# Performance work log

Measured on AMD Instinct MI355X. Metric: run time of the kernel, lower is better.

Reference implementation:

```python
import jax, jax.numpy as jnp
import numpy as np

N = 50000   # nodes
E = 400000  # edges
D = 256     # embedding_dimension
R = 2       # num_relations
NE = 2      # num experts
OUT = 256   # output_size
NEG_SLOPE = 0.01  # nn.LeakyReLU default


def setup_inputs() -> dict:
    key = jax.random.key(0)
    ks = jax.random.split(key, 18)
    s = 0.05
    inp = {
        "des": jax.random.normal(ks[0], (N, 128), jnp.float32),
        "tweet": jax.random.normal(ks[1], (N, 64), jnp.float32),
        "num_prop": jax.random.normal(ks[2], (N, 32), jnp.float32),
        "cat_prop": jax.random.normal(ks[3], (N, 32), jnp.float32),
        "edge_index": jax.random.randint(ks[4], (2, E), 0, N, jnp.int64),
        "edge_type": jax.random.randint(ks[5], (E,), 0, R, jnp.int64),
        # linear_relu_input
        "W_in": jax.random.normal(ks[6], (D, D), jnp.float32) * s,
        "b_in": jnp.zeros((D,), jnp.float32),
        # RGCNConv (shared across the two calls)
        "W_rel": jax.random.normal(ks[7], (R, D, D), jnp.float32) * s,
        "W_root": jax.random.normal(ks[8], (D, D), jnp.float32) * s,
        "b_rgcn": jnp.zeros((D,), jnp.float32),
        # MoE gate + experts (MLP: D -> D -> OUT)
        "w_gate": jax.random.normal(ks[9], (D, NE), jnp.float32) * s,
        "We1": jax.random.normal(ks[10], (NE, D, D), jnp.float32) * s,
        "be1": jnp.zeros((NE, D), jnp.float32),
        "We2": jax.random.normal(ks[11], (NE, D, OUT), jnp.float32) * s,
        "be2": jnp.zeros((NE, OUT), jnp.float32),
    }
    return inp


def _rgcn(x, W_rel, W_root, b, src, dst, edge_type):
    # per-relation node transform, then gather per edge; mean-aggregate per (node, relation)
    h = jnp.einsum('nd,rdh->rnh', x, W_rel)          # (R, N, D)
    msg = h[edge_type, src]                           # (E, D)
    seg = dst * R + edge_type                         # combined (node, relation) segment id
    sums = jax.ops.segment_sum(msg, seg, num_segments=N * R)
    cnt = jax.ops.segment_sum(jnp.ones((E,), msg.dtype), seg, num_segments=N * R)
    agg = sums / jnp.maximum(cnt, 1.0)[:, None]       # per-relation mean (0 if no edges)
    agg = agg.reshape(N, R, -1).sum(axis=1)           # sum over relations
    return x @ W_root + b + agg


def _moe(x, w_gate, We1, be1, We2, be2, k=1):
    # clean (eval) top-k gating: softmax over the top-k logits, scattered into zeros
    logits = x @ w_gate                               # (N, NE)
    top_vals, top_idx = jax.lax.top_k(logits, k)
    gate_vals = jax.nn.softmax(top_vals, axis=-1)     # k=1 -> weight 1.0
    gates = jnp.zeros_like(logits).at[jnp.arange(x.shape[0])[:, None], top_idx].set(gate_vals)
    # compute all experts densely (zero gates annihilate unselected experts)
    h1 = jnp.einsum('nd,edh->enh', x, We1) + be1[:, None, :]
    h1 = jnp.where(h1 >= 0, h1, NEG_SLOPE * h1)       # LeakyReLU
    ye = jnp.einsum('enh,eho->eno', h1, We2) + be2[:, None, :]
    return jnp.einsum('ne,eno->no', gates, ye)


def reference(des, tweet, num_prop, cat_prop, edge_index, edge_type,
              W_in, b_in, W_rel, W_root, b_rgcn, w_gate, We1, be1, We2, be2):
    src, dst = edge_index[0], edge_index[1]
    x = jnp.concatenate((des, tweet, num_prop, cat_prop), axis=1)  # (N, D)
    x = jax.nn.selu(x @ W_in + b_in)
    x = _rgcn(x, W_rel, W_root, b_rgcn, src, dst, edge_type)
    # dropout is identity in eval mode
    x = _rgcn(x, W_rel, W_root, b_rgcn, src, dst, edge_type)
    y = _moe(x, w_gate, We1, be1, We2, be2, k=1)
    return y
```

## Files before the change

kernel.cpp:

```cpp
#include <hip/hip_runtime.h>
#include <cstddef>

static constexpr int N_NODES = 50000;
static constexpr int N_EDGES = 400000;
static constexpr int D = 256;
static constexpr int R = 2;
static constexpr int M_PAD = 50048;
static constexpr int CAP = 32;
static constexpr int NSEG = N_NODES * R;

typedef _Float16 f16x8 __attribute__((ext_vector_type(8)));
typedef float f32x4 __attribute__((ext_vector_type(4)));

__device__ __forceinline__ unsigned short f2h(float f) {
    _Float16 h = (_Float16)f;
    return *(unsigned short*)&h;
}
__device__ __forceinline__ float h2f(unsigned short u) {
    _Float16 h = *(_Float16*)&u;
    return (float)h;
}

#define GLOAD16(g, l)                                                          \
    __builtin_amdgcn_global_load_lds(                                          \
        (const __attribute__((address_space(1))) void*)(g),                    \
        (__attribute__((address_space(3))) void*)(l), 16, 0, 0)

struct SSlab { const float* x; int xstr; int kstart; int mload; };
struct SArgs {
    SSlab sl[4];
    int nslab;
    const unsigned short* wt;
    int Ktot;
    int M;
    const float* bias;
    void* out;
};

template<int ACT>
__global__ __launch_bounds__(256, 2)
void sgemm(SArgs a) {
    __shared__ unsigned short As[2][128 * 32];
    __shared__ unsigned short Bs[2][128 * 32];
    const int tid  = threadIdx.x;
    const int wave = tid >> 6, lane = tid & 63;
    const int wm = wave >> 1, wn = wave & 1;
    const int row0 = blockIdx.x * 128;
    const int n0   = blockIdx.y * 128;

    const int arow  = tid >> 1;
    const int ahalf = tid & 1;
    const int br_   = tid >> 2;
    const int bg_   = tid & 3;

    const int gk   = lane >> 4;
    const int frow = lane & 15;
    const int fslot = (gk ^ ((frow >> 1) & 3)) << 3;

    f32x4 acc0[4][4] = {};
    f32x4 accC[4][4] = {};

    for (int ks = 0; ks < a.Ktot; ks += 32) {
        int s = a.nslab - 1;
        while (s > 0 && ks < a.sl[s].kstart) --s;
        const float* xb = a.sl[s].x;
        const int xstr  = a.sl[s].xstr;
        const int kloc  = ks - a.sl[s].kstart;
        const int mload = a.sl[s].mload;

        float ev[16];
        {
            const int gr = row0 + arow;
            if (gr < mload) {
                const float* ap = xb + (size_t)gr * xstr + kloc + ahalf * 16;
                *(float4*)&ev[0]  = ((const float4*)ap)[0];
                *(float4*)&ev[4]  = ((const float4*)ap)[1];
                *(float4*)&ev[8]  = ((const float4*)ap)[2];
                *(float4*)&ev[12] = ((const float4*)ap)[3];
            } else {
                #pragma unroll
                for (int j = 0; j < 16; ++j) ev[j] = 0.f;
            }
        }

        __syncthreads();

        #pragma unroll
        for (int p = 0; p < 2; ++p) {
            #pragma unroll
            for (int q = 0; q < 2; ++q) {
                const int r = q * 64 + br_;
                const int gsrc = (bg_ ^ ((r >> 1) & 3)) << 3;
                GLOAD16(a.wt + (size_t)p * 256 * a.Ktot + (size_t)(n0 + r) * a.Ktot + ks + gsrc,
                        &Bs[p][(q * 64 + wave * 16) * 32]);
            }
        }

        {
            const int sswz = (arow >> 1) & 3;
            #pragma unroll
            for (int g = 0; g < 2; ++g) {
                union { f16x8 v; _Float16 h[8]; } p1, p2;
                #pragma unroll
                for (int j = 0; j < 8; ++j) {
                    const float v = ev[g * 8 + j];
                    const _Float16 h1 = (_Float16)v;
                    const float r1 = (v - (float)h1) * 2048.0f;
                    p1.h[j] = h1; p2.h[j] = (_Float16)r1;
                }
                const int slot = ((ahalf * 2 + g) ^ sswz) << 3;
                *(f16x8*)&As[0][arow * 32 + slot] = p1.v;
                *(f16x8*)&As[1][arow * 32 + slot] = p2.v;
            }
        }

        __syncthreads();

        f16x8 bq[4][2];
        #pragma unroll
        for (int n = 0; n < 4; ++n) {
            const int rr = wn * 64 + n * 16 + frow;
            #pragma unroll
            for (int p = 0; p < 2; ++p)
                bq[n][p] = *(const f16x8*)&Bs[p][rr * 32 + fslot];
        }
        #pragma unroll
        for (int m = 0; m < 4; ++m) {
            const int rr = wm * 64 + m * 16 + frow;
            const f16x8 a1 = *(const f16x8*)&As[0][rr * 32 + fslot];
            const f16x8 a2 = *(const f16x8*)&As[1][rr * 32 + fslot];
            #pragma unroll
            for (int n = 0; n < 4; ++n) {
                acc0[m][n] = __builtin_amdgcn_mfma_f32_16x16x32_f16(a1, bq[n][0], acc0[m][n], 0, 0, 0);
                accC[m][n] = __builtin_amdgcn_mfma_f32_16x16x32_f16(a1, bq[n][1], accC[m][n], 0, 0, 0);
                accC[m][n] = __builtin_amdgcn_mfma_f32_16x16x32_f16(a2, bq[n][0], accC[m][n], 0, 0, 0);
            }
        }
    }

    const int erow = (lane >> 4) * 4;
    const int ecol = lane & 15;
    #pragma unroll
    for (int m = 0; m < 4; ++m) {
        #pragma unroll
        for (int r = 0; r < 4; ++r) {
            const int grow = row0 + wm * 64 + m * 16 + erow + r;
            if (grow >= a.M) continue;
            #pragma unroll
            for (int n = 0; n < 4; ++n) {
                const int gcol = n0 + wn * 64 + n * 16 + ecol;
                float v = acc0[m][n][r] + accC[m][n][r] * (1.0f / 2048.0f) + a.bias[gcol];
                if (ACT == 1) {
                    const float scale = 1.0507009873554804934f;
                    const float alpha = 1.6732632423543772848f;
                    v = (v > 0.f) ? scale * v : scale * alpha * (expf(v) - 1.f);
                }
                ((float*)a.out)[(size_t)grow * 256 + gcol] = v;
            }
        }
    }
}

struct HSlab { const void* x; int xstr; int kstart; };
struct HArgs {
    HSlab sl[3];
    int nslab;
    const unsigned short* wt;
    int Ktot, M;
    const float* bias;
    const int* sel;
    const int* perm;
    const int* c01;
    void* out;
    int ldc;
};

template<int ACT, bool MASK, bool SELB, bool OUTF16, bool A32, bool EZ, bool PERM>
__global__ __launch_bounds__(256, 2)
void hgemm(HArgs a) {
    __shared__ unsigned short As[128 * 64];
    __shared__ unsigned short Bs[128 * 64];
    const int tid  = threadIdx.x;
    const int wave = tid >> 6, lane = tid & 63;
    const int wm = wave >> 1, wn = wave & 1;
    const int row0 = blockIdx.x * 128;
    const int n0   = blockIdx.y * 128;
    const int ex   = EZ ? (int)blockIdx.z : 0;
    const unsigned short* wt = a.wt + (size_t)ex * 65536;
    const float* bias = a.bias + ex * 256;

    int cntE = 0, base = 0;
    if (PERM) {
        const int c0 = a.c01[0];
        cntE = (ex == 0) ? c0 : a.M - c0;
        base = (ex == 0) ? 0 : c0;
        if (row0 >= cntE) return;
    }

    const int srow = lane >> 3;
    const int scol = ((lane & 7) ^ (lane >> 3)) << 3;
    const int arow  = tid >> 1;
    const int ahalf = tid & 1;

    f32x4 acc[4][4] = {};

    for (int k0 = 0; k0 < a.Ktot; k0 += 64) {
        int s = a.nslab - 1;
        while (s > 0 && k0 < a.sl[s].kstart) --s;
        const int kloc = k0 - a.sl[s].kstart;
        const int xstr = a.sl[s].xstr;

        float ev[32];
        if (A32) {
            const float* xp = (const float*)a.sl[s].x;
            const float* ap = xp + (size_t)(row0 + arow) * xstr + kloc + ahalf * 32;
            #pragma unroll
            for (int q = 0; q < 8; ++q)
                *(float4*)&ev[q * 4] = ((const float4*)ap)[q];
        }

        __syncthreads();

        if (!A32) {
            const unsigned short* xp = (const unsigned short*)a.sl[s].x;
            #pragma unroll
            for (int i = 0; i < 4; ++i) {
                const int r = wave * 32 + i * 8;
                int lr = row0 + r + srow;
                if (PERM) lr = a.perm[base + (lr < cntE ? lr : cntE - 1)];
                GLOAD16(xp + (size_t)lr * xstr + kloc + scol, &As[r * 64]);
            }
        }
        #pragma unroll
        for (int i = 0; i < 4; ++i) {
            const int r = wave * 32 + i * 8;
            GLOAD16(wt + (size_t)(n0 + r + srow) * a.Ktot + k0 + scol, &Bs[r * 64]);
        }
        if (A32) {
            #pragma unroll
            for (int gi = 0; gi < 4; ++gi) {
                const int sgr = ahalf * 4 + gi;
                union { f16x8 v; _Float16 h[8]; } pk;
                #pragma unroll
                for (int j = 0; j < 8; ++j) pk.h[j] = (_Float16)ev[gi * 8 + j];
                *(f16x8*)&As[arow * 64 + ((sgr ^ (arow & 7)) << 3)] = pk.v;
            }
        }

        __syncthreads();

        #pragma unroll
        for (int kk = 0; kk < 2; ++kk) {
            const int gkk = kk * 4 + (lane >> 4);
            f16x8 af[4], bfr[4];
            #pragma unroll
            for (int m = 0; m < 4; ++m) {
                const int rr = wm * 64 + m * 16 + (lane & 15);
                af[m] = *(const f16x8*)&As[rr * 64 + ((gkk ^ (rr & 7)) << 3)];
            }
            #pragma unroll
            for (int n = 0; n < 4; ++n) {
                const int rr = wn * 64 + n * 16 + (lane & 15);
                bfr[n] = *(const f16x8*)&Bs[rr * 64 + ((gkk ^ (rr & 7)) << 3)];
            }
            #pragma unroll
            for (int m = 0; m < 4; ++m)
                #pragma unroll
                for (int n = 0; n < 4; ++n)
                    acc[m][n] = __builtin_amdgcn_mfma_f32_16x16x32_f16(
                        af[m], bfr[n], acc[m][n], 0, 0, 0);
        }
    }

    const int erow = (lane >> 4) * 4;
    const int ecol = lane & 15;
    #pragma unroll
    for (int m = 0; m < 4; ++m) {
        #pragma unroll
        for (int r = 0; r < 4; ++r) {
            const int grow = row0 + wm * 64 + m * 16 + erow + r;
            if (PERM) { if (grow >= cntE) continue; }
            else      { if (grow >= a.M) continue; }
            const int orow = PERM ? a.perm[base + grow] : grow;
            int sv = 0;
            if (MASK || SELB) sv = a.sel[orow];
            #pragma unroll
            for (int n = 0; n < 4; ++n) {
                const int gcol = n0 + wn * 64 + n * 16 + ecol;
                const float b = SELB ? a.bias[sv * 256 + gcol] : bias[gcol];
                float v = acc[m][n][r] + b;
                if (ACT == 2) v = (v >= 0.f) ? v : 0.01f * v;
                if (MASK && sv != ex) v = 0.f;
                const size_t oidx = (size_t)orow * a.ldc + ((EZ && !PERM) ? ex * 256 : 0) + gcol;
                if (OUTF16) ((unsigned short*)a.out)[oidx] = f2h(v);
                else        ((float*)a.out)[oidx] = v;
            }
        }
    }
}

__global__ __launch_bounds__(256)
void csr_build(const int* __restrict__ ei, const int* __restrict__ et,
               int* cnt, int* slots) {
    const int e = blockIdx.x * 256 + threadIdx.x;
    if (e >= N_EDGES) return;
    const int src = ei[e];
    const int dst = ei[N_EDGES + e];
    const int seg = dst * R + et[e];
    const int slot = atomicAdd(&cnt[seg], 1);
    if (slot < CAP) slots[(size_t)seg * CAP + slot] = src;
}

__global__ __launch_bounds__(256)
void aggregate(const float* __restrict__ X, const int* __restrict__ cnt,
               const int* __restrict__ slots, float* __restrict__ Ab,
               int seg0, int nseg) {
    const int w = blockIdx.x * 4 + (threadIdx.x >> 6);
    if (w >= nseg) return;
    const int lane = threadIdx.x & 63;
    const int s = seg0 + w;
    const int m = min(cnt[s], CAP);
    const int* sl = slots + (size_t)s * CAP;
    float4 acc = make_float4(0.f, 0.f, 0.f, 0.f);
    for (int i = 0; i < m; ++i) {
        const float4 v = *(const float4*)(X + (size_t)sl[i] * 256 + lane * 4);
        acc.x += v.x; acc.y += v.y; acc.z += v.z; acc.w += v.w;
    }
    const float inv = (m > 0) ? 1.0f / (float)m : 0.0f;
    acc.x *= inv; acc.y *= inv; acc.z *= inv; acc.w *= inv;
    *(float4*)(Ab + (size_t)(w >> 1) * 512 + (w & 1) * 256 + lane * 4) = acc;
}

__global__ __launch_bounds__(256)
void agg_h(const unsigned short* __restrict__ Xh, const int* __restrict__ cnt,
           const int* __restrict__ slots, unsigned short* __restrict__ Abh) {
    const int w = blockIdx.x * 4 + (threadIdx.x >> 6);
    if (w >= NSEG) return;
    const int lane = threadIdx.x & 63;
    const int m = min(cnt[w], CAP);
    const int* sl = slots + (size_t)w * CAP;
    float ac[4] = {};
    for (int i = 0; i < m; ++i) {
        const ushort4 v = *(const ushort4*)(Xh + (size_t)sl[i] * 256 + lane * 4);
        ac[0] += h2f(v.x); ac[1] += h2f(v.y); ac[2] += h2f(v.z); ac[3] += h2f(v.w);
    }
    const float inv = (m > 0) ? 1.0f / (float)m : 0.0f;
    ushort4 o = make_ushort4(f2h(ac[0] * inv), f2h(ac[1] * inv),
                             f2h(ac[2] * inv), f2h(ac[3] * inv));
    *(ushort4*)(Abh + (size_t)(w >> 1) * 512 + (w & 1) * 256 + lane * 4) = o;
}

__global__ __launch_bounds__(256)
void fold1(const float* __restrict__ W_root, const float* __restrict__ W_rel,
           const float* __restrict__ b_rg, const float* __restrict__ wg,
           float* __restrict__ wfold, float* __restrict__ c3) {
    const int idx = blockIdx.x * 256 + threadIdx.x;
    if (idx < 1536) {
        const int d = idx / 6, jj = idx % 6, c = jj >> 1, j = jj & 1;
        const float* row = (c == 0) ? W_root + (size_t)d * 256
                                    : W_rel + (size_t)(c - 1) * 65536 + (size_t)d * 256;
        float s = 0.f;
        for (int e = 0; e < 256; ++e) s += row[e] * wg[e * 2 + j];
        wfold[idx] = s;
    } else if (idx < 1538) {
        const int j = idx - 1536;
        float s = 0.f;
        for (int e = 0; e < 256; ++e) s += b_rg[e] * wg[e * 2 + j];
        c3[j] = s;
    }
}

__global__ __launch_bounds__(256)
void fold2(const float* __restrict__ W_root, const float* __restrict__ W_rel,
           const float* __restrict__ b_rg, const float* __restrict__ wfold,
           float* __restrict__ W6, float* __restrict__ cb) {
    const int idx = blockIdx.x * 256 + threadIdx.x;
    if (idx < 4608) {
        const int k = idx / 6, j = idx % 6;
        const float* row = (k < 256) ? W_root + (size_t)k * 256
                                     : W_rel + (size_t)(k - 256) * 256;
        float s = 0.f;
        for (int d = 0; d < 256; ++d) s += row[d] * wfold[d * 6 + j];
        W6[idx] = s;
    } else if (idx < 4614) {
        const int j = idx - 4608;
        float s = 0.f;
        for (int d = 0; d < 256; ++d) s += b_rg[d] * wfold[d * 6 + j];
        cb[j] = s;
    }
}

__global__ __launch_bounds__(256)
void vu_kernel(const float* __restrict__ X1, const float* __restrict__ Ab,
               const float* __restrict__ W6, float* __restrict__ VU, int M) {
    __shared__ float wl[768 * 6];
    for (int i = threadIdx.x; i < 768 * 6; i += 256) wl[i] = W6[i];
    __syncthreads();
    const int wave = threadIdx.x >> 6, lane = threadIdx.x & 63;
    const int n = blockIdx.x * 4 + wave;
    if (n >= M) return;
    const float4 xv = ((const float4*)(X1 + (size_t)n * 256))[lane];
    const float4 a0 = ((const float4*)(Ab + (size_t)n * 512))[lane];
    const float4 a1 = ((const float4*)(Ab + (size_t)n * 512))[lane + 64];
    const float xa[12] = {xv.x, xv.y, xv.z, xv.w, a0.x, a0.y, a0.z, a0.w,
                          a1.x, a1.y, a1.z, a1.w};
    float z[6] = {};
    #pragma unroll
    for (int t = 0; t < 3; ++t)
        #pragma unroll
        for (int i = 0; i < 4; ++i) {
            const int k = t * 256 + lane * 4 + i;
            #pragma unroll
            for (int j = 0; j < 6; ++j) z[j] = fmaf(xa[t * 4 + i], wl[k * 6 + j], z[j]);
        }
    #pragma unroll
    for (int off = 32; off; off >>= 1)
        #pragma unroll
        for (int j = 0; j < 6; ++j) z[j] += __shfl_down(z[j], off, 64);
    if (lane == 0) {
        #pragma unroll
        for (int j = 0; j < 6; ++j) VU[(size_t)n * 6 + j] = z[j];
    }
}

__global__ __launch_bounds__(256)
void u_gate(const float* __restrict__ VU, const int* __restrict__ cnt,
            const int* __restrict__ slots, const float* __restrict__ cb,
            const float* __restrict__ c3, int* __restrict__ sel, int M) {
    const int n = blockIdx.x * 256 + threadIdx.x;
    if (n >= M) return;
    float z0 = VU[(size_t)n * 6 + 0] + cb[0] + c3[0];
    float z1 = VU[(size_t)n * 6 + 1] + cb[1] + c3[1];
    #pragma unroll
    for (int r = 0; r < 2; ++r) {
        const int seg = n * 2 + r;
        const int m = min(cnt[seg], CAP);
        if (m > 0) {
            const int* sl = slots + (size_t)seg * CAP;
            float s0 = 0.f, s1 = 0.f;
            for (int i = 0; i < m; ++i) {
                const int src = sl[i];
                s0 += VU[(size_t)src * 6 + 2 + 2 * r];
                s1 += VU[(size_t)src * 6 + 3 + 2 * r];
            }
            const float inv = 1.0f / (float)m;
            z0 += s0 * inv + cb[2 + 2 * r];
            z1 += s1 * inv + cb[3 + 2 * r];
        }
    }
    sel[n] = (z1 > z0) ? 1 : 0;
}

__global__ __launch_bounds__(256)
void build_perm(const int* __restrict__ sel, int* __restrict__ perm, int* c01) {
    const int n = blockIdx.x * 256 + threadIdx.x;
    if (n >= N_NODES) return;
    if (sel[n] == 0) perm[atomicAdd(&c01[0], 1)] = n;
    else             perm[N_NODES - 1 - atomicAdd(&c01[1], 1)] = n;
}

__global__ __launch_bounds__(256)
void wconv2(const float* __restrict__ src, unsigned short* __restrict__ dst) {
    const int i = blockIdx.x * 256 + threadIdx.x;
    const int k = i >> 8, n = i & 255;
    const float v = src[i];
    const _Float16 h1 = (_Float16)v;
    const float r1 = (v - (float)h1) * 2048.0f;
    dst[(size_t)n * 256 + k] = f2h(v);
    dst[65536 + (size_t)n * 256 + k] = *(unsigned short*)&h1 == 0 ? f2h(r1) : f2h(r1);
}

struct WJH { const float* src[8]; unsigned short* dst[8]; int stride[8]; int koff[8]; };
__global__ __launch_bounds__(256)
void wconv_h(WJH j) {
    const int job = blockIdx.y;
    const int i = blockIdx.x * 256 + threadIdx.x;
    const int k = i >> 8, n = i & 255;
    j.dst[job][(size_t)n * j.stride[job] + j.koff[job] + k] = f2h(j.src[job][i]);
}

extern "C" void kernel_launch(void* const* d_in, const int* in_sizes, int n_in,
                              void* d_out, int out_size, void* d_ws, size_t ws_size,
                              hipStream_t stream) {
    const float* des    = (const float*)d_in[0];
    const float* twt    = (const float*)d_in[1];
    const float* nump   = (const float*)d_in[2];
    const float* catp   = (const float*)d_in[3];
    const int*   ei     = (const int*)d_in[4];
    const int*   et     = (const int*)d_in[5];
    const float* W_in   = (const float*)d_in[6];
    const float* b_in   = (const float*)d_in[7];
    const float* W_rel  = (const float*)d_in[8];
    const float* W_root = (const float*)d_in[9];
    const float* b_rg   = (const float*)d_in[10];
    const float* w_gate = (const float*)d_in[11];
    const float* We1    = (const float*)d_in[12];
    const float* be1    = (const float*)d_in[13];
    const float* We2    = (const float*)d_in[14];
    const float* be2    = (const float*)d_in[15];

    char* ws = (char*)d_ws;
    size_t off = 0;
    auto alloc = [&](size_t bytes) { char* p = ws + off; off += (bytes + 255) & ~(size_t)255; return p; };
    float* X1f  = (float*)alloc((size_t)M_PAD * 256 * 4);
    char*  regA = alloc((size_t)M_PAD * 512 * 4);
    unsigned short* X2h = (unsigned short*)alloc((size_t)M_PAD * 256 * 2);
    float* VU   = (float*)alloc((size_t)N_NODES * 6 * 4);
    int*   cnt  = (int*)alloc((size_t)NSEG * 4);
    int*   sel  = (int*)alloc((size_t)N_NODES * 4);
    int*   perm = (int*)alloc((size_t)N_NODES * 4);
    int*   c01  = (int*)alloc(256);
    int*   slots= (int*)alloc((size_t)NSEG * CAP * 4);
    unsigned short* wt_in2 = (unsigned short*)alloc((size_t)2 * 65536 * 2);
    unsigned short* wt_rg  = (unsigned short*)alloc((size_t)256 * 768 * 2);
    unsigned short* wt_e1  = (unsigned short*)alloc((size_t)2 * 65536 * 2);
    unsigned short* wt_e2  = (unsigned short*)alloc((size_t)2 * 65536 * 2);
    float* wfold = (float*)alloc(256 * 6 * 4);
    float* c3    = (float*)alloc(8);
    float* W6    = (float*)alloc(768 * 6 * 4);
    float* cb    = (float*)alloc(24);

    float* Ab1f = (float*)regA;
    unsigned short* Ab2h = (unsigned short*)regA;
    unsigned short* H    = (unsigned short*)(regA + (size_t)M_PAD * 512 * 2);
    unsigned short* X3h  = (unsigned short*)X1f;

    const dim3 blk(256);

    hipMemsetAsync(cnt, 0, (size_t)NSEG * 4, stream);
    hipMemsetAsync(c01, 0, 8, stream);
    csr_build<<<(N_EDGES + 255) / 256, blk, 0, stream>>>(ei, et, cnt, slots);
    wconv2<<<256, blk, 0, stream>>>(W_in, wt_in2);
    {
        WJH j{};
        j.src[0] = W_root;         j.dst[0] = wt_rg;         j.stride[0] = 768; j.koff[0] = 0;
        j.src[1] = W_rel;          j.dst[1] = wt_rg;         j.stride[1] = 768; j.koff[1] = 256;
        j.src[2] = W_rel + 65536;  j.dst[2] = wt_rg;         j.stride[2] = 768; j.koff[2] = 512;
        j.src[3] = We1;            j.dst[3] = wt_e1;         j.stride[3] = 256; j.koff[3] = 0;
        j.src[4] = We1 + 65536;    j.dst[4] = wt_e1 + 65536; j.stride[4] = 256; j.koff[4] = 0;
        j.src[5] = We2;            j.dst[5] = wt_e2;         j.stride[5] = 256; j.koff[5] = 0;
        j.src[6] = We2 + 65536;    j.dst[6] = wt_e2 + 65536; j.stride[6] = 256; j.koff[6] = 0;
        wconv_h<<<dim3(256, 7), blk, 0, stream>>>(j);
    }
    fold1<<<7, blk, 0, stream>>>(W_root, W_rel, b_rg, w_gate, wfold, c3);
    fold2<<<19, blk, 0, stream>>>(W_root, W_rel, b_rg, wfold, W6, cb);

    {
        SArgs g{};
        g.sl[0] = {des,  128, 0,   N_NODES};
        g.sl[1] = {twt,  64,  128, N_NODES};
        g.sl[2] = {nump, 32,  192, N_NODES};
        g.sl[3] = {catp, 32,  224, N_NODES};
        g.nslab = 4; g.wt = wt_in2; g.Ktot = 256; g.M = N_NODES;
        g.bias = b_in; g.out = X1f;
        hipLaunchKernelGGL((sgemm<1>), dim3(391, 2), blk, 0, stream, g);
    }

    aggregate<<<(NSEG + 3) / 4, blk, 0, stream>>>(X1f, cnt, slots, Ab1f, 0, NSEG);

    vu_kernel<<<(N_NODES + 3) / 4, blk, 0, stream>>>(X1f, Ab1f, W6, VU, N_NODES);
    u_gate<<<(N_NODES + 255) / 256, blk, 0, stream>>>(VU, cnt, slots, cb, c3, sel, N_NODES);
    build_perm<<<(N_NODES + 255) / 256, blk, 0, stream>>>(sel, perm, c01);

    {
        HArgs g{};
        g.sl[0] = {X1f,        256, 0};
        g.sl[1] = {Ab1f,       512, 256};
        g.sl[2] = {Ab1f + 256, 512, 512};
        g.nslab = 3; g.wt = wt_rg; g.Ktot = 768; g.M = N_NODES;
        g.bias = b_rg; g.out = X2h; g.ldc = 256;
        hipLaunchKernelGGL((hgemm<0, false, false, true, true, false, false>),
                           dim3(391, 2), blk, 0, stream, g);
    }

    agg_h<<<(NSEG + 3) / 4, blk, 0, stream>>>(X2h, cnt, slots, Ab2h);

    {
        HArgs g{};
        g.sl[0] = {X2h,        256, 0};
        g.sl[1] = {Ab2h,       512, 256};
        g.sl[2] = {Ab2h + 256, 512, 512};
        g.nslab = 3; g.wt = wt_rg; g.Ktot = 768; g.M = N_NODES;
        g.bias = b_rg; g.out = X3h; g.ldc = 256;
        hipLaunchKernelGGL((hgemm<0, false, false, true, false, false, false>),
                           dim3(391, 2), blk, 0, stream, g);
    }

    {
        HArgs g{};
        g.sl[0] = {X3h, 256, 0};
        g.nslab = 1; g.wt = wt_e1; g.Ktot = 256; g.M = N_NODES;
        g.bias = be1; g.perm = perm; g.c01 = c01; g.out = H; g.ldc = 256;
        hipLaunchKernelGGL((hgemm<2, false, false, true, false, true, true>),
                           dim3(391, 2, 2), blk, 0, stream, g);
    }

    {
        HArgs g{};
        g.sl[0] = {H, 256, 0};
        g.nslab = 1; g.wt = wt_e2; g.Ktot = 256; g.M = N_NODES;
        g.bias = be2; g.perm = perm; g.c01 = c01; g.out = d_out; g.ldc = 256;
        hipLaunchKernelGGL((hgemm<0, false, false, false, false, true, true>),
                           dim3(391, 2, 2), blk, 0, stream, g);
    }
}
```

Before: 476.6 us.

## Double-buffer LDS tiles in sgemm/hgemm and unroll gather aggregation by two

```diff
diff --git a/kernel.cpp b/kernel.cpp
--- a/kernel.cpp
+++ b/kernel.cpp
@@ -40,8 +40,8 @@
 template<int ACT>
 __global__ __launch_bounds__(256, 2)
 void sgemm(SArgs a) {
-    __shared__ unsigned short As[2][128 * 32];
-    __shared__ unsigned short Bs[2][128 * 32];
+    __shared__ unsigned short As[2][2][128 * 32];
+    __shared__ unsigned short Bs[2][2][128 * 32];
     const int tid  = threadIdx.x;
     const int wave = tid >> 6, lane = tid & 63;
     const int wm = wave >> 1, wn = wave & 1;
@@ -57,34 +57,28 @@
     const int frow = lane & 15;
     const int fslot = (gk ^ ((frow >> 1) & 3)) << 3;
 
-    f32x4 acc0[4][4] = {};
-    f32x4 accC[4][4] = {};
-
-    for (int ks = 0; ks < a.Ktot; ks += 32) {
+    const int NT = a.Ktot / 32;
+    float ev[16];
+
+    auto loadA = [&](int t) {
+        const int ks = t * 32;
         int s = a.nslab - 1;
         while (s > 0 && ks < a.sl[s].kstart) --s;
-        const float* xb = a.sl[s].x;
-        const int xstr  = a.sl[s].xstr;
-        const int kloc  = ks - a.sl[s].kstart;
-        const int mload = a.sl[s].mload;
-
-        float ev[16];
-        {
-            const int gr = row0 + arow;
-            if (gr < mload) {
-                const float* ap = xb + (size_t)gr * xstr + kloc + ahalf * 16;
-                *(float4*)&ev[0]  = ((const float4*)ap)[0];
-                *(float4*)&ev[4]  = ((const float4*)ap)[1];
-                *(float4*)&ev[8]  = ((const float4*)ap)[2];
-                *(float4*)&ev[12] = ((const float4*)ap)[3];
-            } else {
-                #pragma unroll
-                for (int j = 0; j < 16; ++j) ev[j] = 0.f;
-            }
-        }
-
-        __syncthreads();
-
+        const int gr = row0 + arow;
+        if (gr < a.sl[s].mload) {
+            const float* ap = a.sl[s].x + (size_t)gr * a.sl[s].xstr
+                              + (ks - a.sl[s].kstart) + ahalf * 16;
+            *(float4*)&ev[0]  = ((const float4*)ap)[0];
+            *(float4*)&ev[4]  = ((const float4*)ap)[1];
+            *(float4*)&ev[8]  = ((const float4*)ap)[2];
+            *(float4*)&ev[12] = ((const float4*)ap)[3];
+        } else {
+            #pragma unroll
+            for (int j = 0; j < 16; ++j) ev[j] = 0.f;
+        }
+    };
+    auto stageB = [&](int buf, int t) {
+        const int ks = t * 32;
         #pragma unroll
         for (int p = 0; p < 2; ++p) {
             #pragma unroll
@@ -92,29 +86,39 @@
                 const int r = q * 64 + br_;
                 const int gsrc = (bg_ ^ ((r >> 1) & 3)) << 3;
                 GLOAD16(a.wt + (size_t)p * 256 * a.Ktot + (size_t)(n0 + r) * a.Ktot + ks + gsrc,
-                        &Bs[p][(q * 64 + wave * 16) * 32]);
-            }
-        }
-
-        {
-            const int sswz = (arow >> 1) & 3;
-            #pragma unroll
-            for (int g = 0; g < 2; ++g) {
-                union { f16x8 v; _Float16 h[8]; } p1, p2;
-                #pragma unroll
-                for (int j = 0; j < 8; ++j) {
-                    const float v = ev[g * 8 + j];
-                    const _Float16 h1 = (_Float16)v;
-                    const float r1 = (v - (float)h1) * 2048.0f;
-                    p1.h[j] = h1; p2.h[j] = (_Float16)r1;
-                }
-                const int slot = ((ahalf * 2 + g) ^ sswz) << 3;
-                *(f16x8*)&As[0][arow * 32 + slot] = p1.v;
-                *(f16x8*)&As[1][arow * 32 + slot] = p2.v;
-            }
-        }
-
-        __syncthreads();
+                        &Bs[buf][p][(q * 64 + wave * 16) * 32]);
+            }
+        }
+    };
+    auto writeA = [&](int buf) {
+        const int sswz = (arow >> 1) & 3;
+        #pragma unroll
+        for (int g = 0; g < 2; ++g) {
+            union { f16x8 v; _Float16 h[8]; } p1, p2;
+            #pragma unroll
+            for (int j = 0; j < 8; ++j) {
+                const float v = ev[g * 8 + j];
+                const _Float16 h1 = (_Float16)v;
+                const float r1 = (v - (float)h1) * 2048.0f;
+                p1.h[j] = h1; p2.h[j] = (_Float16)r1;
+            }
+            const int slot = ((ahalf * 2 + g) ^ sswz) << 3;
+            *(f16x8*)&As[buf][0][arow * 32 + slot] = p1.v;
+            *(f16x8*)&As[buf][1][arow * 32 + slot] = p2.v;
+        }
+    };
+
+    f32x4 acc0[4][4] = {};
+    f32x4 accC[4][4] = {};
+
+    loadA(0);
+    stageB(0, 0);
+    writeA(0);
+    __syncthreads();
+
+    for (int t = 0; t < NT; ++t) {
+        const int cur = t & 1, nxt = cur ^ 1;
+        if (t + 1 < NT) { loadA(t + 1); stageB(nxt, t + 1); }
 
         f16x8 bq[4][2];
         #pragma unroll
@@ -122,13 +126,13 @@
             const int rr = wn * 64 + n * 16 + frow;
             #pragma unroll
             for (int p = 0; p < 2; ++p)
-                bq[n][p] = *(const f16x8*)&Bs[p][rr * 32 + fslot];
+                bq[n][p] = *(const f16x8*)&Bs[cur][p][rr * 32 + fslot];
         }
         #pragma unroll
         for (int m = 0; m < 4; ++m) {
             const int rr = wm * 64 + m * 16 + frow;
-            const f16x8 a1 = *(const f16x8*)&As[0][rr * 32 + fslot];
-            const f16x8 a2 = *(const f16x8*)&As[1][rr * 32 + fslot];
+            const f16x8 a1 = *(const f16x8*)&As[cur][0][rr * 32 + fslot];
+            const f16x8 a2 = *(const f16x8*)&As[cur][1][rr * 32 + fslot];
             #pragma unroll
             for (int n = 0; n < 4; ++n) {
                 acc0[m][n] = __builtin_amdgcn_mfma_f32_16x16x32_f16(a1, bq[n][0], acc0[m][n], 0, 0, 0);
@@ -136,6 +140,8 @@
                 accC[m][n] = __builtin_amdgcn_mfma_f32_16x16x32_f16(a2, bq[n][0], accC[m][n], 0, 0, 0);
             }
         }
+        __syncthreads();
+        if (t + 1 < NT) { writeA(nxt); __syncthreads(); }
     }
 
     const int erow = (lane >> 4) * 4;
@@ -178,8 +184,8 @@
 template<int ACT, bool MASK, bool SELB, bool OUTF16, bool A32, bool EZ, bool PERM>
 __global__ __launch_bounds__(256, 2)
 void hgemm(HArgs a) {
-    __shared__ unsigned short As[128 * 64];
-    __shared__ unsigned short Bs[128 * 64];
+    __shared__ unsigned short As[2][128 * 64];
+    __shared__ unsigned short Bs[2][128 * 64];
     const int tid  = threadIdx.x;
     const int wave = tid >> 6, lane = tid & 63;
     const int wm = wave >> 1, wn = wave & 1;
@@ -202,52 +208,67 @@
     const int arow  = tid >> 1;
     const int ahalf = tid & 1;
 
-    f32x4 acc[4][4] = {};
-
-    for (int k0 = 0; k0 < a.Ktot; k0 += 64) {
+    const int NT = a.Ktot / 64;
+    float ev[32];
+
+    auto loadA32 = [&](int t) {
+        const int k0 = t * 64;
         int s = a.nslab - 1;
         while (s > 0 && k0 < a.sl[s].kstart) --s;
+        const float* xp = (const float*)a.sl[s].x;
+        const float* ap = xp + (size_t)(row0 + arow) * a.sl[s].xstr
+                          + (k0 - a.sl[s].kstart) + ahalf * 32;
+        #pragma unroll
+        for (int q = 0; q < 8; ++q)
+            *(float4*)&ev[q * 4] = ((const float4*)ap)[q];
+    };
+    auto stageA = [&](int buf, int t) {
+        const int k0 = t * 64;
+        int s = a.nslab - 1;
+        while (s > 0 && k0 < a.sl[s].kstart) --s;
+        const unsigned short* xp = (const unsigned short*)a.sl[s].x;
         const int kloc = k0 - a.sl[s].kstart;
         const int xstr = a.sl[s].xstr;
-
-        float ev[32];
-        if (A32) {
-            const float* xp = (const float*)a.sl[s].x;
-            const float* ap = xp + (size_t)(row0 + arow) * xstr + kloc + ahalf * 32;
-            #pragma unroll
-            for (int q = 0; q < 8; ++q)
-                *(float4*)&ev[q * 4] = ((const float4*)ap)[q];
-        }
-
-        __syncthreads();
-
-        if (!A32) {
-            const unsigned short* xp = (const unsigned short*)a.sl[s].x;
-            #pragma unroll
-            for (int i = 0; i < 4; ++i) {
-                const int r = wave * 32 + i * 8;
-                int lr = row0 + r + srow;
-                if (PERM) lr = a.perm[base + (lr < cntE ? lr : cntE - 1)];
-                GLOAD16(xp + (size_t)lr * xstr + kloc + scol, &As[r * 64]);
-            }
-        }
         #pragma unroll
         for (int i = 0; i < 4; ++i) {
             const int r = wave * 32 + i * 8;
-            GLOAD16(wt + (size_t)(n0 + r + srow) * a.Ktot + k0 + scol, &Bs[r * 64]);
-        }
-        if (A32) {
-            #pragma unroll
-            for (int gi = 0; gi < 4; ++gi) {
-                const int sgr = ahalf * 4 + gi;
-                union { f16x8 v; _Float16 h[8]; } pk;
-                #pragma unroll
-                for (int j = 0; j < 8; ++j) pk.h[j] = (_Float16)ev[gi * 8 + j];
-                *(f16x8*)&As[arow * 64 + ((sgr ^ (arow & 7)) << 3)] = pk.v;
-            }
-        }
-
-        __syncthreads();
+            int lr = row0 + r + srow;
+            if (PERM) lr = a.perm[base + (lr < cntE ? lr : cntE - 1)];
+            GLOAD16(xp + (size_t)lr * xstr + kloc + scol, &As[buf][r * 64]);
+        }
+    };
+    auto stageB = [&](int buf, int t) {
+        const int k0 = t * 64;
+        #pragma unroll
+        for (int i = 0; i < 4; ++i) {
+            const int r = wave * 32 + i * 8;
+            GLOAD16(wt + (size_t)(n0 + r + srow) * a.Ktot + k0 + scol, &Bs[buf][r * 64]);
+        }
+    };
+    auto writeA32 = [&](int buf) {
+        #pragma unroll
+        for (int gi = 0; gi < 4; ++gi) {
+            const int sgr = ahalf * 4 + gi;
+            union { f16x8 v; _Float16 h[8]; } pk;
+            #pragma unroll
+            for (int j = 0; j < 8; ++j) pk.h[j] = (_Float16)ev[gi * 8 + j];
+            *(f16x8*)&As[buf][arow * 64 + ((sgr ^ (arow & 7)) << 3)] = pk.v;
+        }
+    };
+
+    f32x4 acc[4][4] = {};
+
+    if (A32) loadA32(0); else stageA(0, 0);
+    stageB(0, 0);
+    if (A32) writeA32(0);
+    __syncthreads();
+
+    for (int t = 0; t < NT; ++t) {
+        const int cur = t & 1, nxt = cur ^ 1;
+        if (t + 1 < NT) {
+            if (A32) loadA32(t + 1); else stageA(nxt, t + 1);
+            stageB(nxt, t + 1);
+        }
 
         #pragma unroll
         for (int kk = 0; kk < 2; ++kk) {
@@ -256,12 +277,12 @@
             #pragma unroll
             for (int m = 0; m < 4; ++m) {
                 const int rr = wm * 64 + m * 16 + (lane & 15);
-                af[m] = *(const f16x8*)&As[rr * 64 + ((gkk ^ (rr & 7)) << 3)];
+                af[m] = *(const f16x8*)&As[cur][rr * 64 + ((gkk ^ (rr & 7)) << 3)];
             }
             #pragma unroll
             for (int n = 0; n < 4; ++n) {
                 const int rr = wn * 64 + n * 16 + (lane & 15);
-                bfr[n] = *(const f16x8*)&Bs[rr * 64 + ((gkk ^ (rr & 7)) << 3)];
+                bfr[n] = *(const f16x8*)&Bs[cur][rr * 64 + ((gkk ^ (rr & 7)) << 3)];
             }
             #pragma unroll
             for (int m = 0; m < 4; ++m)
@@ -270,6 +291,8 @@
                     acc[m][n] = __builtin_amdgcn_mfma_f32_16x16x32_f16(
                         af[m], bfr[n], acc[m][n], 0, 0, 0);
         }
+        __syncthreads();
+        if (A32 && t + 1 < NT) { writeA32(nxt); __syncthreads(); }
     }
 
     const int erow = (lane >> 4) * 4;
@@ -322,7 +345,14 @@
     const int m = min(cnt[s], CAP);
     const int* sl = slots + (size_t)s * CAP;
     float4 acc = make_float4(0.f, 0.f, 0.f, 0.f);
-    for (int i = 0; i < m; ++i) {
+    int i = 0;
+    for (; i + 1 < m; i += 2) {
+        const float4 v0 = *(const float4*)(X + (size_t)sl[i] * 256 + lane * 4);
+        const float4 v1 = *(const float4*)(X + (size_t)sl[i + 1] * 256 + lane * 4);
+        acc.x += v0.x + v1.x; acc.y += v0.y + v1.y;
+        acc.z += v0.z + v1.z; acc.w += v0.w + v1.w;
+    }
+    if (i < m) {
         const float4 v = *(const float4*)(X + (size_t)sl[i] * 256 + lane * 4);
         acc.x += v.x; acc.y += v.y; acc.z += v.z; acc.w += v.w;
     }
@@ -340,7 +370,14 @@
     const int m = min(cnt[w], CAP);
     const int* sl = slots + (size_t)w * CAP;
     float ac[4] = {};
-    for (int i = 0; i < m; ++i) {
+    int i = 0;
+    for (; i + 1 < m; i += 2) {
+        const ushort4 v0 = *(const ushort4*)(Xh + (size_t)sl[i] * 256 + lane * 4);
+        const ushort4 v1 = *(const ushort4*)(Xh + (size_t)sl[i + 1] * 256 + lane * 4);
+        ac[0] += h2f(v0.x) + h2f(v1.x); ac[1] += h2f(v0.y) + h2f(v1.y);
+        ac[2] += h2f(v0.z) + h2f(v1.z); ac[3] += h2f(v0.w) + h2f(v1.w);
+    }
+    if (i < m) {
         const ushort4 v = *(const ushort4*)(Xh + (size_t)sl[i] * 256 + lane * 4);
         ac[0] += h2f(v.x); ac[1] += h2f(v.y); ac[2] += h2f(v.z); ac[3] += h2f(v.w);
     }
@@ -467,7 +504,7 @@
     const _Float16 h1 = (_Float16)v;
     const float r1 = (v - (float)h1) * 2048.0f;
     dst[(size_t)n * 256 + k] = f2h(v);
-    dst[65536 + (size_t)n * 256 + k] = *(unsigned short*)&h1 == 0 ? f2h(r1) : f2h(r1);
+    dst[65536 + (size_t)n * 256 + k] = f2h(r1);
 }
 
 struct WJH { const float* src[8]; unsigned short* dst[8]; int stride[8]; int koff[8]; };
```

Result: slower. 490.5 us (median of 4 runs) (+2.9%).
